# Kernel tuning notes

Measured on AMD Instinct MI355X. Metric: run time of the kernel, lower is better.

Reference implementation:

```python
import jax, jax.numpy as jnp
import numpy as np

B, N, M, DQ, DK, DV, H = 8, 1024, 1024, 512, 512, 512, 8
DH = DV // H           # per-head dim (dim_split)
DFF = 4 * DV           # FFN hidden dim
EPS = 1e-5


def _layernorm(x, g, b):
    mu = jnp.mean(x, axis=-1, keepdims=True)
    var = jnp.mean(jnp.square(x - mu), axis=-1, keepdims=True)
    return (x - mu) * jax.lax.rsqrt(var + EPS) * g + b


def setup_inputs() -> dict:
    key = jax.random.key(0)
    ks = jax.random.split(key, 20)
    s = 0.02
    return {
        "Q": jax.random.normal(ks[0], (B, N, DQ), jnp.float32),
        "K": jax.random.normal(ks[1], (B, M, DK), jnp.float32),
        "Wq": jax.random.normal(ks[2], (DV, DQ), jnp.float32) * s,
        "bq": jnp.zeros((DV,), jnp.float32),
        "Wk": jax.random.normal(ks[3], (DV, DK), jnp.float32) * s,
        "bk": jnp.zeros((DV,), jnp.float32),
        "Wv": jax.random.normal(ks[4], (DV, DK), jnp.float32) * s,
        "bv": jnp.zeros((DV,), jnp.float32),
        "W1": jax.random.normal(ks[5], (DFF, DV), jnp.float32) * s,
        "b1": jnp.zeros((DFF,), jnp.float32),
        "W2": jax.random.normal(ks[6], (DFF, DFF), jnp.float32) * s,
        "b2": jnp.zeros((DFF,), jnp.float32),
        "W3": jax.random.normal(ks[7], (DV, DFF), jnp.float32) * s,
        "b3": jnp.zeros((DV,), jnp.float32),
        "g0": jnp.ones((DV,), jnp.float32),
        "beta0": jnp.zeros((DV,), jnp.float32),
        "g1": jnp.ones((DV,), jnp.float32),
        "beta1": jnp.zeros((DV,), jnp.float32),
    }


def reference(Q, K, Wq, bq, Wk, bk, Wv, bv, W1, b1, W2, b2, W3, b3, g0, beta0, g1, beta1):
    # projections (torch Linear: x @ W.T + b)
    Qp = Q @ Wq.T + bq            # [B, N, DV]
    Kp = K @ Wk.T + bk            # [B, M, DV]
    Vp = K @ Wv.T + bv            # [B, M, DV]

    # split heads: [B, S, DV] -> [B, S, H, DH]
    Qh = Qp.reshape(B, N, H, DH)
    Kh = Kp.reshape(B, M, H, DH)
    Vh = Vp.reshape(B, M, H, DH)

    # scaled dot-product attention (scale = sqrt(head_dim))
    A = jnp.einsum("bnhd,bmhd->bhnm", Qh, Kh) / jnp.sqrt(jnp.float32(DH))
    A = jax.nn.softmax(A, axis=-1)
    O = jnp.einsum("bhnm,bmhd->bnhd", A, Vh).reshape(B, N, DV)

    # residual with projected Q, then LN
    O = _layernorm(O + Qp, g0, beta0)

    # FFN: Linear->ReLU->Linear->ReLU->Linear (num_hidden_layers=2)
    h = jax.nn.relu(O @ W1.T + b1)
    h = jax.nn.relu(h @ W2.T + b2)
    Off = h @ W3.T + b3

    return _layernorm(O + Off, g1, beta1)
```

## Files before the change

### kernel.cpp

```cpp
#include <hip/hip_runtime.h>


typedef __bf16 bf16_t;
typedef __bf16 bf16x8 __attribute__((ext_vector_type(8)));
typedef __bf16 bf16x4 __attribute__((ext_vector_type(4)));
typedef __bf16 bf16x2 __attribute__((ext_vector_type(2)));
typedef float  f32x4  __attribute__((ext_vector_type(4)));
typedef float  f32x16 __attribute__((ext_vector_type(16)));
typedef int    i32x4_t __attribute__((ext_vector_type(4)));
typedef int    i32x8_t __attribute__((ext_vector_type(8)));

__device__ __forceinline__ f32x4 mfma16(bf16x8 a, bf16x8 b, f32x4 c) {
  return __builtin_amdgcn_mfma_f32_16x16x32_bf16(a, b, c, 0, 0, 0);
}

__device__ __forceinline__ void gload_lds16(const void* g, void* l) {
  __builtin_amdgcn_global_load_lds((const __attribute__((address_space(1))) void*)g,
                                   (__attribute__((address_space(3))) void*)l,
                                   16, 0, 0);
}

__device__ __forceinline__ unsigned char to_fp8(float v) {
  return (unsigned char)(__builtin_amdgcn_cvt_pk_fp8_f32(v, v, 0, false) & 0xff);
}

__global__ __launch_bounds__(256) void cast_all(
    const float* __restrict__ Q, const float* __restrict__ K,
    const float* __restrict__ Wq, const float* __restrict__ Wk,
    const float* __restrict__ Wv, const float* __restrict__ W1,
    const float* __restrict__ W2, const float* __restrict__ W3,
    bf16_t* Qb, bf16_t* Kb, bf16_t* Wqb, bf16_t* Wkb, bf16_t* Wvb,
    bf16_t* W1b, unsigned char* W2q, bf16_t* W3b)
{
  long i = ((long)blockIdx.x * 256 + threadIdx.x) * 4;
  if (i >= 10223616L && i < 14417920L) {
    long o = i - 10223616L;
    float4 v = *(const float4*)(W2 + o);
    unsigned int lo = __builtin_amdgcn_cvt_pk_fp8_f32(v.x, v.y, 0, false);
    unsigned int hi = __builtin_amdgcn_cvt_pk_fp8_f32(v.z, v.w, 0, false);
    *(unsigned int*)(W2q + o) = (lo & 0xffffu) | (hi << 16);
    return;
  }
  const float* s; bf16_t* d; long o;
  if      (i <  4194304L) { s = Q;  d = Qb;  o = i;             }
  else if (i <  8388608L) { s = K;  d = Kb;  o = i - 4194304L;  }
  else if (i <  8650752L) { s = Wq; d = Wqb; o = i - 8388608L;  }
  else if (i <  8912896L) { s = Wk; d = Wkb; o = i - 8650752L;  }
  else if (i <  9175040L) { s = Wv; d = Wvb; o = i - 8912896L;  }
  else if (i < 10223616L) { s = W1; d = W1b; o = i - 9175040L;  }
  else                    { s = W3; d = W3b; o = i - 14417920L; }
  float4 v = *(const float4*)(s + o);
  bf16x4 w;
  w[0] = (bf16_t)v.x; w[1] = (bf16_t)v.y; w[2] = (bf16_t)v.z; w[3] = (bf16_t)v.w;
  *(bf16x4*)(d + o) = w;
}

template <int BM, bool RELU, bool VTEPI>
__device__ __forceinline__ void gemm_core(
    const bf16_t* __restrict__ A, const bf16_t* __restrict__ W,
    const float* __restrict__ bias, float* __restrict__ Cf,
    bf16_t* __restrict__ Cb, unsigned char* __restrict__ C8,
    bf16_t* __restrict__ VTout,
    float bscale, int N, int K, int lda, int ldb, int bx, int by)
{
  constexpr int WM = (BM == 128) ? 2 : 1;
  constexpr int WN = 4 / WM;
  constexpr int FI = 4;
  constexpr int FJ = 128 / (WN * 16);
  constexpr int CN = 128 / WN;
  constexpr int AISS = BM / 32;
  constexpr int SM_AB = (BM + 128) * 64 * 2;
  constexpr int SM_TS = 128 * 132 * 2;
  constexpr int SMEM = (VTEPI && SM_TS > SM_AB) ? SM_TS : SM_AB;

  __shared__ __align__(16) char smem[SMEM];
  bf16_t* As = (bf16_t*)smem;
  bf16_t* Bs = (bf16_t*)(smem + BM * 64 * 2);

  const int tid  = threadIdx.x;
  const int wave = tid >> 6, lane = tid & 63;
  const int lq   = lane & 15, quad = lane >> 4;
  const int wm   = (WM == 2) ? (wave & 1) : 0;
  const int wn   = (WM == 2) ? (wave >> 1) : wave;
  const long row0 = (long)bx * BM;
  const long col0 = (long)by * 128;

  const int sr = tid >> 3;
  const int cg = (tid & 7) ^ (sr & 7);
  const bf16_t* ag = A + (row0 + sr) * (long)lda + cg * 8;
  const bf16_t* bg = W + (col0 + sr) * (long)ldb + cg * 8;
  char* asD = (char*)As + wave * 1024;
  char* bsD = (char*)Bs + wave * 1024;

  const int off0 = (quad ^ (lq & 7)) * 8;
  const bf16_t* aR0 = As + (wm * 64 + lq) * 64 + off0;
  const bf16_t* aR1 = As + (wm * 64 + lq) * 64 + (off0 ^ 32);
  const bf16_t* bR0 = Bs + (wn * CN + lq) * 64 + off0;
  const bf16_t* bR1 = Bs + (wn * CN + lq) * 64 + (off0 ^ 32);

  f32x4 acc[FI][FJ];
#pragma unroll
  for (int i = 0; i < FI; i++)
#pragma unroll
    for (int j = 0; j < FJ; j++) acc[i][j] = (f32x4){0.f, 0.f, 0.f, 0.f};

  const long arows32 = 32L * lda;
  const long brows32 = 32L * ldb;
  for (int k0 = 0; k0 < K; k0 += 64) {
    __syncthreads();
#pragma unroll
    for (int is = 0; is < AISS; is++)
      gload_lds16(ag + is * arows32 + k0, asD + is * 4096);
#pragma unroll
    for (int is = 0; is < 4; is++)
      gload_lds16(bg + is * brows32 + k0, bsD + is * 4096);
    __syncthreads();
    bf16x8 af[FI], bw[FJ];
#pragma unroll
    for (int i = 0; i < FI; i++) af[i] = *(const bf16x8*)(aR0 + i * 1024);
#pragma unroll
    for (int j = 0; j < FJ; j++) bw[j] = *(const bf16x8*)(bR0 + j * 1024);
#pragma unroll
    for (int i = 0; i < FI; i++)
#pragma unroll
      for (int j = 0; j < FJ; j++)
        acc[i][j] = mfma16(af[i], bw[j], acc[i][j]);
#pragma unroll
    for (int i = 0; i < FI; i++) af[i] = *(const bf16x8*)(aR1 + i * 1024);
#pragma unroll
    for (int j = 0; j < FJ; j++) bw[j] = *(const bf16x8*)(bR1 + j * 1024);
#pragma unroll
    for (int i = 0; i < FI; i++)
#pragma unroll
      for (int j = 0; j < FJ; j++)
        acc[i][j] = mfma16(af[i], bw[j], acc[i][j]);
  }

  float bc[FJ];
#pragma unroll
  for (int j = 0; j < FJ; j++)
    bc[j] = bias ? bias[col0 + wn * CN + j * 16 + lq] : 0.f;

  if (VTEPI && VTout) {
    bf16_t* Ts = (bf16_t*)smem;
    __syncthreads();
#pragma unroll
    for (int i = 0; i < FI; i++)
#pragma unroll
      for (int j = 0; j < FJ; j++) {
        bf16x4 pv;
#pragma unroll
        for (int r = 0; r < 4; r++) pv[r] = (bf16_t)(acc[i][j][r] + bc[j]);
        *(bf16x4*)(Ts + (wn * CN + j * 16 + lq) * 132 + wm * 64 + i * 16 + quad * 4) = pv;
      }
    __syncthreads();
    const int b  = bx >> 3;
    const int mb = (bx & 7) * 128;
    const int h0 = by * 2;
    const int dd = tid >> 4;
    const int mc = (tid & 15) * 8;
#pragma unroll
    for (int p = 0; p < 8; p++) {
      const int d = dd + p * 16;
      bf16x8 v = *(const bf16x8*)(Ts + d * 132 + mc);
      *(bf16x8*)(VTout + ((long)(b * 8 + h0 + (d >> 6))) * 65536
                 + (d & 63) * 1024 + mb + mc) = v;
    }
    return;
  }

  const long rb = row0 + wm * 64 + quad * 4;
  const long cb = col0 + wn * CN + lq;
#pragma unroll
  for (int i = 0; i < FI; i++)
#pragma unroll
    for (int j = 0; j < FJ; j++)
#pragma unroll
      for (int r = 0; r < 4; r++) {
        float v = acc[i][j][r] + bc[j];
        if (RELU) v = fmaxf(v, 0.f);
        long idx = (rb + i * 16 + r) * (long)N + cb + j * 16;
        if (Cf) Cf[idx] = v;
        if (Cb) Cb[idx] = (bf16_t)(v * bscale);
        if (C8) C8[idx] = to_fp8(v);
      }
}

template <int BM, bool RELU>
__global__ __launch_bounds__(256) void gemm_bt(
    const bf16_t* __restrict__ A, const bf16_t* __restrict__ W,
    const float* __restrict__ bias, float* __restrict__ Cf,
    bf16_t* __restrict__ Cb, unsigned char* __restrict__ C8,
    float bscale, int N, int K)
{
  gemm_core<BM, RELU, false>(A, W, bias, Cf, Cb, C8, nullptr, bscale,
                             N, K, K, K, blockIdx.x, blockIdx.y);
}

__global__ __launch_bounds__(256) void ffn3_splitk(
    const bf16_t* __restrict__ H2, const bf16_t* __restrict__ W3b,
    bf16_t* __restrict__ Off01)
{
  const int z = blockIdx.z;
  gemm_core<128, false, false>(H2 + z * 1024, W3b + z * 1024, nullptr,
                               nullptr, Off01 + (long)z * 4194304, nullptr,
                               nullptr, 1.0f, 512, 1024, 2048, 2048,
                               blockIdx.x, blockIdx.y);
}

__global__ __launch_bounds__(256) void proj3(
    const bf16_t* __restrict__ Qb, const bf16_t* __restrict__ Kb,
    const bf16_t* __restrict__ Wqb, const bf16_t* __restrict__ Wkb,
    const bf16_t* __restrict__ Wvb,
    const float* __restrict__ bq, const float* __restrict__ bk,
    const float* __restrict__ bv,
    bf16_t* Qpb, bf16_t* Kpb, bf16_t* VT)
{
  const int z = blockIdx.z;
  const bf16_t* A  = (z == 0) ? Qb : Kb;
  const bf16_t* Wt = (z == 0) ? Wqb : ((z == 1) ? Wkb : Wvb);
  const float* bias = (z == 0) ? bq : ((z == 1) ? bk : bv);
  bf16_t* Cb = (z == 0) ? Qpb : ((z == 1) ? Kpb : nullptr);
  bf16_t* VTout = (z == 2) ? VT : nullptr;
  const float sc = (z == 1) ? 0.125f : 1.0f;
  gemm_core<128, false, true>(A, Wt, bias, nullptr, Cb, nullptr, VTout, sc,
                              512, 512, 512, 512, blockIdx.x, blockIdx.y);
}

__global__ __launch_bounds__(256) void ffn2_fp8(
    const unsigned char* __restrict__ H1, const unsigned char* __restrict__ W2,
    const float* __restrict__ bias, bf16_t* __restrict__ C)
{
  __shared__ unsigned char As[16384];
  __shared__ unsigned char Bs[16384];
  const int tid = threadIdx.x;
  const int wave = tid >> 6, lane = tid & 63;
  const int wm = wave & 1, wn = wave >> 1;
  const int m = lane & 31, h = lane >> 5;
  const long row0 = (long)blockIdx.x * 128;
  const long col0 = (long)blockIdx.y * 128;

  const int sr = tid >> 3;
  const int cg = (tid & 7) ^ (sr & 7);
  const unsigned char* ag = H1 + (row0 + sr) * 2048 + cg * 16;
  const unsigned char* bg = W2 + (col0 + sr) * 2048 + cg * 16;
  char* asD = (char*)As + wave * 1024;
  char* bsD = (char*)Bs + wave * 1024;

  const int ar0 = wm * 64 + m, ar1 = ar0 + 32;
  const int br0 = wn * 64 + m, br1 = br0 + 32;

  f32x16 acc[2][2];
#pragma unroll
  for (int mi = 0; mi < 2; mi++)
#pragma unroll
    for (int nj = 0; nj < 2; nj++)
#pragma unroll
      for (int r = 0; r < 16; r++) acc[mi][nj][r] = 0.f;

  for (int k0 = 0; k0 < 2048; k0 += 128) {
    __syncthreads();
#pragma unroll
    for (int is = 0; is < 4; is++)
      gload_lds16(ag + is * 65536 + k0, asD + is * 4096);
#pragma unroll
    for (int is = 0; is < 4; is++)
      gload_lds16(bg + is * 65536 + k0, bsD + is * 4096);
    __syncthreads();
#pragma unroll
    for (int ks = 0; ks < 2; ks++) {
      const int c0 = ks * 4 + h * 2;
      i32x8_t a[2], b[2];
#pragma unroll
      for (int mi = 0; mi < 2; mi++) {
        const int r = mi ? ar1 : ar0;
        i32x4_t lo = *(const i32x4_t*)(As + r * 128 + ((c0    ) ^ (r & 7)) * 16);
        i32x4_t hi = *(const i32x4_t*)(As + r * 128 + ((c0 + 1) ^ (r & 7)) * 16);
        a[mi][0] = lo[0]; a[mi][1] = lo[1]; a[mi][2] = lo[2]; a[mi][3] = lo[3];
        a[mi][4] = hi[0]; a[mi][5] = hi[1]; a[mi][6] = hi[2]; a[mi][7] = hi[3];
      }
#pragma unroll
      for (int nj = 0; nj < 2; nj++) {
        const int r = nj ? br1 : br0;
        i32x4_t lo = *(const i32x4_t*)(Bs + r * 128 + ((c0    ) ^ (r & 7)) * 16);
        i32x4_t hi = *(const i32x4_t*)(Bs + r * 128 + ((c0 + 1) ^ (r & 7)) * 16);
        b[nj][0] = lo[0]; b[nj][1] = lo[1]; b[nj][2] = lo[2]; b[nj][3] = lo[3];
        b[nj][4] = hi[0]; b[nj][5] = hi[1]; b[nj][6] = hi[2]; b[nj][7] = hi[3];
      }
#pragma unroll
      for (int mi = 0; mi < 2; mi++)
#pragma unroll
        for (int nj = 0; nj < 2; nj++)
          acc[mi][nj] = __builtin_amdgcn_mfma_scale_f32_32x32x64_f8f6f4(
              a[mi], b[nj], acc[mi][nj], 0, 0,
              0, 0x7f7f7f7f, 0, 0x7f7f7f7f);
    }
  }

  float bc[2];
  bc[0] = bias[col0 + wn * 64 + m];
  bc[1] = bias[col0 + wn * 64 + 32 + m];
#pragma unroll
  for (int mi = 0; mi < 2; mi++)
#pragma unroll
    for (int nj = 0; nj < 2; nj++)
#pragma unroll
      for (int reg = 0; reg < 16; reg++) {
        const int rl = (reg & 3) + 8 * (reg >> 2) + 4 * h;
        float v = fmaxf(acc[mi][nj][reg] + bc[nj], 0.f);
        C[(row0 + wm * 64 + mi * 32 + rl) * 2048 + col0 + wn * 64 + nj * 32 + m]
            = (bf16_t)v;
      }
}

__global__ __launch_bounds__(256) void attn(
    const bf16_t* __restrict__ Qp, const bf16_t* __restrict__ Kp,
    const bf16_t* __restrict__ VT, bf16_t* __restrict__ O)
{
  const int d0 = blockIdx.x;
  const int j  = d0 >> 3;
  const int g  = (d0 & 7) * 8 + (j >> 4);
  const int qb = j & 15;
  const int h  = g & 7, b = g >> 3;

  const int tid = threadIdx.x;
  const int wave = tid >> 6, lane = tid & 63;
  const int lq = lane & 15, quad = lane >> 4;

  __shared__ bf16_t Ks[2][8192];
  __shared__ bf16_t VTs[2][8192];
  __shared__ bf16_t Ps[4][16 * 72];

  const long bh = (long)b * 1024;
  const int qrow = qb * 64 + wave * 16 + lq;

  const bf16_t* qptr = Qp + (bh + qrow) * 512 + h * 64 + quad * 8;
  const bf16x8 qf0 = *(const bf16x8*)qptr;
  const bf16x8 qf1 = *(const bf16x8*)(qptr + 32);

  f32x4 oacc[4];
#pragma unroll
  for (int t = 0; t < 4; t++) oacc[t] = (f32x4){0.f, 0.f, 0.f, 0.f};
  float l_i = 0.f;

  const int sr = tid >> 3;
  const int cg = (tid & 7) ^ (sr & 7);
  const bf16_t* kg  = Kp + bh * 512 + h * 64;
  const bf16_t* vtg = VT + ((long)b * 8 + h) * 65536;
  const int off0 = (quad ^ (lq & 7)) * 8;

  auto stage = [&](int m0, int bi) {
    char* ksDst = (char*)(Ks[bi]) + wave * 1024;
    char* vtDst = (char*)(VTs[bi]) + wave * 1024;
#pragma unroll
    for (int s = 0; s < 2; s++) {
      gload_lds16(kg + (long)(m0 + s * 64 + sr) * 512 + cg * 8,      ksDst + s * 8192);
      gload_lds16(kg + (long)(m0 + s * 64 + sr + 32) * 512 + cg * 8, ksDst + s * 8192 + 4096);
      gload_lds16(vtg + (long)sr * 1024 + m0 + s * 64 + cg * 8,        vtDst + s * 8192);
      gload_lds16(vtg + (long)(sr + 32) * 1024 + m0 + s * 64 + cg * 8, vtDst + s * 8192 + 4096);
    }
  };

  stage(0, 0);

  for (int t = 0; t < 8; ++t) {
    const int cur = t & 1;
    if (t < 7) {
      stage((t + 1) * 128, cur ^ 1);
      asm volatile("s_waitcnt vmcnt(8)" ::: "memory");
    } else {
      asm volatile("s_waitcnt vmcnt(0)" ::: "memory");
    }
    __builtin_amdgcn_s_barrier();
    __builtin_amdgcn_sched_barrier(0);

    const bf16_t* Kc = Ks[cur];
    const bf16_t* Vc = VTs[cur];

    f32x4 st[8];
#pragma unroll
    for (int tt = 0; tt < 8; tt++) {
      const bf16_t* kb = Kc + (tt >> 2) * 4096 + ((tt & 3) * 16 + lq) * 64;
      bf16x8 ka0 = *(const bf16x8*)(kb + off0);
      bf16x8 ka1 = *(const bf16x8*)(kb + (off0 ^ 32));
      f32x4 s = (f32x4){0.f, 0.f, 0.f, 0.f};
      s = mfma16(ka0, qf0, s);
      s = mfma16(ka1, qf1, s);
      st[tt] = s;
    }
    float lsum = 0.f;
#pragma unroll
    for (int tt = 0; tt < 8; tt++)
#pragma unroll
      for (int r = 0; r < 4; r++) {
        float p = __expf(st[tt][r]);
        st[tt][r] = p;
        lsum += p;
      }
    lsum += __shfl_xor(lsum, 16, 64);
    lsum += __shfl_xor(lsum, 32, 64);
    l_i += lsum;

    bf16_t* pw = &Ps[wave][0];
#pragma unroll
    for (int hh = 0; hh < 2; hh++) {
#pragma unroll
      for (int tt = 0; tt < 4; tt++) {
        bf16x4 pv;
#pragma unroll
        for (int r = 0; r < 4; r++) pv[r] = (bf16_t)st[hh * 4 + tt][r];
        *(bf16x4*)(pw + lq * 72 + tt * 16 + quad * 4) = pv;
      }
#pragma unroll
      for (int ks = 0; ks < 2; ks++) {
        bf16x8 pb = *(const bf16x8*)(pw + lq * 72 + ks * 32 + quad * 8);
#pragma unroll
        for (int dt = 0; dt < 4; dt++) {
          const bf16_t* vb = Vc + hh * 4096 + (dt * 16 + lq) * 64;
          bf16x8 va = *(const bf16x8*)(vb + (ks ? (off0 ^ 32) : off0));
          oacc[dt] = mfma16(va, pb, oacc[dt]);
        }
      }
    }

    __builtin_amdgcn_sched_barrier(0);
    __builtin_amdgcn_s_barrier();
  }

  const float inv = 1.f / l_i;
  bf16_t* op = O + (bh + qrow) * 512 + h * 64 + quad * 4;
#pragma unroll
  for (int dt = 0; dt < 4; dt++) {
    bf16x4 v;
#pragma unroll
    for (int r = 0; r < 4; r++) v[r] = (bf16_t)(oacc[dt][r] * inv);
    *(bf16x4*)(op + dt * 16) = v;
  }
}

__device__ __forceinline__ float2 ld2(const float* p, long row, int tid) {
  return ((const float2*)(p + row * 512))[tid];
}
__device__ __forceinline__ float2 ld2(const bf16_t* p, long row, int tid) {
  bf16x2 v = *(const bf16x2*)(p + row * 512 + tid * 2);
  return make_float2((float)v[0], (float)v[1]);
}

__device__ __forceinline__ void ln_finish(
    float x0, float x1, const float* g, const float* be, int tid,
    int wave, int lane, float* of, bf16_t* ob, long row)
{
  float s = x0 + x1, ss = x0 * x0 + x1 * x1;
#pragma unroll
  for (int off = 1; off < 64; off <<= 1) {
    s  += __shfl_xor(s,  off, 64);
    ss += __shfl_xor(ss, off, 64);
  }
  __shared__ float sm[8];
  if (lane == 0) { sm[wave] = s; sm[4 + wave] = ss; }
  __syncthreads();
  s  = sm[0] + sm[1] + sm[2] + sm[3];
  ss = sm[4] + sm[5] + sm[6] + sm[7];
  const float mu = s * (1.f / 512.f);
  const float var = ss * (1.f / 512.f) - mu * mu;
  const float rs = rsqrtf(var + 1e-5f);
  const float2 gg = ((const float2*)g)[tid];
  const float2 bb = ((const float2*)be)[tid];
  const float o0 = (x0 - mu) * rs * gg.x + bb.x;
  const float o1 = (x1 - mu) * rs * gg.y + bb.y;
  if (of) ((float2*)(of + row * 512))[tid] = make_float2(o0, o1);
  if (ob) {
    bf16x2 t; t[0] = (bf16_t)o0; t[1] = (bf16_t)o1;
    *(bf16x2*)(ob + row * 512 + tid * 2) = t;
  }
}

__global__ __launch_bounds__(256) void ln_res(
    const bf16_t* __restrict__ A, const bf16_t* __restrict__ Bv,
    const float* __restrict__ g, const float* __restrict__ be,
    bf16_t* __restrict__ ob)
{
  const int row = blockIdx.x, tid = threadIdx.x;
  const float2 va = ld2(A,  (long)row, tid);
  const float2 vb = ld2(Bv, (long)row, tid);
  ln_finish(va.x + vb.x, va.y + vb.y, g, be, tid, tid >> 6, tid & 63,
            nullptr, ob, row);
}

__global__ __launch_bounds__(256) void ln_res3(
    const bf16_t* __restrict__ X, const bf16_t* __restrict__ O0,
    const bf16_t* __restrict__ O1, const float* __restrict__ bias,
    const float* __restrict__ g, const float* __restrict__ be,
    float* __restrict__ of)
{
  const int row = blockIdx.x, tid = threadIdx.x;
  const float2 vx = ld2(X,  (long)row, tid);
  const float2 v0 = ld2(O0, (long)row, tid);
  const float2 v1 = ld2(O1, (long)row, tid);
  const float2 vb = ((const float2*)bias)[tid];
  ln_finish(vx.x + v0.x + v1.x + vb.x, vx.y + v0.y + v1.y + vb.y,
            g, be, tid, tid >> 6, tid & 63, of, nullptr, row);
}

extern "C" void kernel_launch(void* const* d_in, const int* in_sizes, int n_in,
                              void* d_out, int out_size, void* d_ws, size_t ws_size,
                              hipStream_t stream)
{
  const float* Q   = (const float*)d_in[0];
  const float* K   = (const float*)d_in[1];
  const float* Wq  = (const float*)d_in[2];
  const float* bq  = (const float*)d_in[3];
  const float* Wk  = (const float*)d_in[4];
  const float* bk  = (const float*)d_in[5];
  const float* Wv  = (const float*)d_in[6];
  const float* bv  = (const float*)d_in[7];
  const float* W1  = (const float*)d_in[8];
  const float* b1  = (const float*)d_in[9];
  const float* W2  = (const float*)d_in[10];
  const float* b2  = (const float*)d_in[11];
  const float* W3  = (const float*)d_in[12];
  const float* b3  = (const float*)d_in[13];
  const float* g0  = (const float*)d_in[14];
  const float* be0 = (const float*)d_in[15];
  const float* g1  = (const float*)d_in[16];
  const float* be1 = (const float*)d_in[17];

  char* ws = (char*)d_ws;
  bf16_t* Wqb = (bf16_t*)(ws + 0);
  bf16_t* Wkb = (bf16_t*)(ws + 524288);
  bf16_t* Wvb = (bf16_t*)(ws + 1048576);
  bf16_t* W1b = (bf16_t*)(ws + 1572864);
  bf16_t* W3b = (bf16_t*)(ws + 3670016);
  unsigned char* W2q = (unsigned char*)(ws + 5767168);
  bf16_t* Qb  = (bf16_t*)(ws + 14155776);
  bf16_t* Kb  = (bf16_t*)(ws + 22544384);
  bf16_t* Qpb = (bf16_t*)(ws + 30932992);
  bf16_t* Kpb = (bf16_t*)(ws + 39321600);
  bf16_t* VT  = (bf16_t*)(ws + 47710208);
  bf16_t* Of  = (bf16_t*)(ws + 14155776);
  bf16_t* Xb  = (bf16_t*)(ws + 22544384);
  bf16_t* H2  = (bf16_t*)(ws + 30932992);
  unsigned char* H1q = (unsigned char*)(ws + 64487424);
  bf16_t* Off0 = (bf16_t*)(ws + 64487424);
  bf16_t* Off1 = (bf16_t*)(ws + 72876032);
  float*  out = (float*)d_out;

  cast_all<<<15104, 256, 0, stream>>>(Q, K, Wq, Wk, Wv, W1, W2, W3,
                                      Qb, Kb, Wqb, Wkb, Wvb, W1b, W2q, W3b);
  proj3<<<dim3(64, 4, 3), 256, 0, stream>>>(Qb, Kb, Wqb, Wkb, Wvb, bq, bk, bv,
                                            Qpb, Kpb, VT);
  attn<<<dim3(1024, 1, 1), 256, 0, stream>>>(Qpb, Kpb, VT, Of);
  ln_res<<<8192, 256, 0, stream>>>(Of, Qpb, g0, be0, Xb);
  gemm_bt<128, true ><<<dim3(64, 16), 256, 0, stream>>>(Xb, W1b, b1, nullptr, nullptr, H1q, 1.0f, 2048, 512);
  ffn2_fp8<<<dim3(64, 16), 256, 0, stream>>>(H1q, W2q, b2, H2);
  ffn3_splitk<<<dim3(64, 4, 2), 256, 0, stream>>>(H2, W3b, Off0);
  ln_res3<<<8192, 256, 0, stream>>>(Xb, Off0, Off1, b3, g1, be1, out);
}
```

Before: 285.9 us.

## Process two query tiles per attention block to reuse staged K/V

```diff
diff --git a/kernel.cpp b/kernel.cpp
--- a/kernel.cpp
+++ b/kernel.cpp
@@ -319,8 +319,8 @@
 {
   const int d0 = blockIdx.x;
   const int j  = d0 >> 3;
-  const int g  = (d0 & 7) * 8 + (j >> 4);
-  const int qb = j & 15;
+  const int g  = (d0 & 7) * 8 + (j >> 3);
+  const int qb = j & 7;
   const int h  = g & 7, b = g >> 3;
 
   const int tid = threadIdx.x;
@@ -332,16 +332,23 @@
   __shared__ bf16_t Ps[4][16 * 72];
 
   const long bh = (long)b * 1024;
-  const int qrow = qb * 64 + wave * 16 + lq;
-
-  const bf16_t* qptr = Qp + (bh + qrow) * 512 + h * 64 + quad * 8;
-  const bf16x8 qf0 = *(const bf16x8*)qptr;
-  const bf16x8 qf1 = *(const bf16x8*)(qptr + 32);
-
-  f32x4 oacc[4];
-#pragma unroll
-  for (int t = 0; t < 4; t++) oacc[t] = (f32x4){0.f, 0.f, 0.f, 0.f};
-  float l_i = 0.f;
+  const int qrowA = qb * 128 + wave * 16 + lq;
+  const int qrowB = qrowA + 64;
+
+  const bf16_t* qpA = Qp + (bh + qrowA) * 512 + h * 64 + quad * 8;
+  const bf16_t* qpB = Qp + (bh + qrowB) * 512 + h * 64 + quad * 8;
+  const bf16x8 qfA0 = *(const bf16x8*)qpA;
+  const bf16x8 qfA1 = *(const bf16x8*)(qpA + 32);
+  const bf16x8 qfB0 = *(const bf16x8*)qpB;
+  const bf16x8 qfB1 = *(const bf16x8*)(qpB + 32);
+
+  f32x4 oaccA[4], oaccB[4];
+#pragma unroll
+  for (int t = 0; t < 4; t++) {
+    oaccA[t] = (f32x4){0.f, 0.f, 0.f, 0.f};
+    oaccB[t] = (f32x4){0.f, 0.f, 0.f, 0.f};
+  }
+  float lA = 0.f, lB = 0.f;
 
   const int sr = tid >> 3;
   const int cg = (tid & 7) ^ (sr & 7);
@@ -377,29 +384,40 @@
     const bf16_t* Kc = Ks[cur];
     const bf16_t* Vc = VTs[cur];
 
-    f32x4 st[8];
+    f32x4 stA[8], stB[8];
 #pragma unroll
     for (int tt = 0; tt < 8; tt++) {
       const bf16_t* kb = Kc + (tt >> 2) * 4096 + ((tt & 3) * 16 + lq) * 64;
       bf16x8 ka0 = *(const bf16x8*)(kb + off0);
       bf16x8 ka1 = *(const bf16x8*)(kb + (off0 ^ 32));
-      f32x4 s = (f32x4){0.f, 0.f, 0.f, 0.f};
-      s = mfma16(ka0, qf0, s);
-      s = mfma16(ka1, qf1, s);
-      st[tt] = s;
-    }
-    float lsum = 0.f;
+      f32x4 sA = (f32x4){0.f, 0.f, 0.f, 0.f};
+      sA = mfma16(ka0, qfA0, sA);
+      sA = mfma16(ka1, qfA1, sA);
+      stA[tt] = sA;
+      f32x4 sB = (f32x4){0.f, 0.f, 0.f, 0.f};
+      sB = mfma16(ka0, qfB0, sB);
+      sB = mfma16(ka1, qfB1, sB);
+      stB[tt] = sB;
+    }
+
+    float lsA = 0.f, lsB = 0.f;
 #pragma unroll
     for (int tt = 0; tt < 8; tt++)
 #pragma unroll
       for (int r = 0; r < 4; r++) {
-        float p = __expf(st[tt][r]);
-        st[tt][r] = p;
-        lsum += p;
-      }
-    lsum += __shfl_xor(lsum, 16, 64);
-    lsum += __shfl_xor(lsum, 32, 64);
-    l_i += lsum;
+        float pA = __expf(stA[tt][r]);
+        stA[tt][r] = pA;
+        lsA += pA;
+        float pB = __expf(stB[tt][r]);
+        stB[tt][r] = pB;
+        lsB += pB;
+      }
+    lsA += __shfl_xor(lsA, 16, 64);
+    lsA += __shfl_xor(lsA, 32, 64);
+    lA += lsA;
+    lsB += __shfl_xor(lsB, 16, 64);
+    lsB += __shfl_xor(lsB, 32, 64);
+    lB += lsB;
 
     bf16_t* pw = &Ps[wave][0];
 #pragma unroll
@@ -408,7 +426,7 @@
       for (int tt = 0; tt < 4; tt++) {
         bf16x4 pv;
 #pragma unroll
-        for (int r = 0; r < 4; r++) pv[r] = (bf16_t)st[hh * 4 + tt][r];
+        for (int r = 0; r < 4; r++) pv[r] = (bf16_t)stA[hh * 4 + tt][r];
         *(bf16x4*)(pw + lq * 72 + tt * 16 + quad * 4) = pv;
       }
 #pragma unroll
@@ -418,7 +436,27 @@
         for (int dt = 0; dt < 4; dt++) {
           const bf16_t* vb = Vc + hh * 4096 + (dt * 16 + lq) * 64;
           bf16x8 va = *(const bf16x8*)(vb + (ks ? (off0 ^ 32) : off0));
-          oacc[dt] = mfma16(va, pb, oacc[dt]);
+          oaccA[dt] = mfma16(va, pb, oaccA[dt]);
+        }
+      }
+    }
+#pragma unroll
+    for (int hh = 0; hh < 2; hh++) {
+#pragma unroll
+      for (int tt = 0; tt < 4; tt++) {
+        bf16x4 pv;
+#pragma unroll
+        for (int r = 0; r < 4; r++) pv[r] = (bf16_t)stB[hh * 4 + tt][r];
+        *(bf16x4*)(pw + lq * 72 + tt * 16 + quad * 4) = pv;
+      }
+#pragma unroll
+      for (int ks = 0; ks < 2; ks++) {
+        bf16x8 pb = *(const bf16x8*)(pw + lq * 72 + ks * 32 + quad * 8);
+#pragma unroll
+        for (int dt = 0; dt < 4; dt++) {
+          const bf16_t* vb = Vc + hh * 4096 + (dt * 16 + lq) * 64;
+          bf16x8 va = *(const bf16x8*)(vb + (ks ? (off0 ^ 32) : off0));
+          oaccB[dt] = mfma16(va, pb, oaccB[dt]);
         }
       }
     }
@@ -427,14 +465,20 @@
     __builtin_amdgcn_s_barrier();
   }
 
-  const float inv = 1.f / l_i;
-  bf16_t* op = O + (bh + qrow) * 512 + h * 64 + quad * 4;
+  const float invA = 1.f / lA;
+  const float invB = 1.f / lB;
+  bf16_t* opA = O + (bh + qrowA) * 512 + h * 64 + quad * 4;
+  bf16_t* opB = O + (bh + qrowB) * 512 + h * 64 + quad * 4;
 #pragma unroll
   for (int dt = 0; dt < 4; dt++) {
-    bf16x4 v;
-#pragma unroll
-    for (int r = 0; r < 4; r++) v[r] = (bf16_t)(oacc[dt][r] * inv);
-    *(bf16x4*)(op + dt * 16) = v;
+    bf16x4 vA, vB;
+#pragma unroll
+    for (int r = 0; r < 4; r++) {
+      vA[r] = (bf16_t)(oaccA[dt][r] * invA);
+      vB[r] = (bf16_t)(oaccB[dt][r] * invB);
+    }
+    *(bf16x4*)(opA + dt * 16) = vA;
+    *(bf16x4*)(opB + dt * 16) = vB;
   }
 }
 
@@ -549,7 +593,7 @@
                                       Qb, Kb, Wqb, Wkb, Wvb, W1b, W2q, W3b);
   proj3<<<dim3(64, 4, 3), 256, 0, stream>>>(Qb, Kb, Wqb, Wkb, Wvb, bq, bk, bv,
                                             Qpb, Kpb, VT);
-  attn<<<dim3(1024, 1, 1), 256, 0, stream>>>(Qpb, Kpb, VT, Of);
+  attn<<<dim3(512, 1, 1), 256, 0, stream>>>(Qpb, Kpb, VT, Of);
   ln_res<<<8192, 256, 0, stream>>>(Of, Qpb, g0, be0, Xb);
   gemm_bt<128, true ><<<dim3(64, 16), 256, 0, stream>>>(Xb, W1b, b1, nullptr, nullptr, H1q, 1.0f, 2048, 512);
   ffn2_fp8<<<dim3(64, 16), 256, 0, stream>>>(H1q, W2q, b2, H2);
```

New measurement: 268.4 us. 6.1% less time.
